# Optimization experiments

Measured on AMD Instinct MI355X. Metric: run time of the kernel, lower is better.

Reference implementation:

```python
import jax, jax.numpy as jnp
import numpy as np

B, S, H = 64, 2048, 1024

def setup_inputs() -> dict:
    key = jax.random.key(0)
    k1, k2 = jax.random.split(key)
    enc_output = jax.random.normal(k1, (B, S, H), dtype=jnp.float32)
    h_n = jax.random.normal(k2, (B, H), dtype=jnp.float32)
    return {"enc_output": enc_output, "h_n": h_n}

def reference(enc_output, h_n):
    # dec_output: [B, 1, H]
    dec_output = h_n[:, None, :]
    # scores: [B, 1, S] = dec_output @ enc_output^T
    scores = jnp.einsum('bqh,bsh->bqs', dec_output, enc_output)
    attn = jax.nn.softmax(scores, axis=2)  # softmax over S
    # context: [B, 1, H] = attn @ enc_output
    context = jnp.einsum('bqs,bsh->bqh', attn, enc_output)
    # concat decoder state and attention context: [B, 1, 2H]
    return jnp.concatenate((dec_output, context), axis=2)
```

## Files before the change

kernel.cpp:

```cpp
#include <hip/hip_runtime.h>
#include <math.h>


#define BB 64
#define SS 2048
#define HH 1024
#define NCHUNK 32
#define SCHUNK (SS / NCHUNK)
#define NWAVE 4
#define RUN (SCHUNK / NWAVE)

typedef float fvec4 __attribute__((ext_vector_type(4)));

#define WS_ML_OFF ((size_t)BB * NCHUNK * HH)

__global__ __launch_bounds__(256) void attn_partial_kernel(
    const float* __restrict__ enc, const float* __restrict__ hn,
    float* __restrict__ ws)
{
    const int blk   = blockIdx.x;
    const int b     = blk >> 5;
    const int chunk = blk & (NCHUNK - 1);
    const int tid   = threadIdx.x;
    const int wave  = tid >> 6;
    const int lane  = tid & 63;

    const fvec4* hn4 = (const fvec4*)(hn + (size_t)b * HH);
    fvec4 h4[4];
#pragma unroll
    for (int j = 0; j < 4; ++j) h4[j] = hn4[j * 64 + lane];

    const fvec4* enc4 = (const fvec4*)(enc + (size_t)b * SS * HH);

    float m = -INFINITY;
    float l = 0.0f;
    fvec4 acc[4];
#pragma unroll
    for (int j = 0; j < 4; ++j) acc[j] = (fvec4)(0.f, 0.f, 0.f, 0.f);

    const int rowbase = chunk * SCHUNK + wave * RUN;
    const int start   = (blk * 53 + wave * 29) & (RUN - 1);

    for (int i = 0; i < RUN; ++i) {
        const int r = rowbase + ((start + i) & (RUN - 1));
        const fvec4* row = enc4 + (size_t)r * (HH / 4);
        fvec4 e[4];
#pragma unroll
        for (int j = 0; j < 4; ++j)
            e[j] = __builtin_nontemporal_load(&row[j * 64 + lane]);

        float d = 0.0f;
#pragma unroll
        for (int j = 0; j < 4; ++j) {
            d += e[j].x * h4[j].x + e[j].y * h4[j].y
               + e[j].z * h4[j].z + e[j].w * h4[j].w;
        }
#pragma unroll
        for (int off = 32; off > 0; off >>= 1)
            d += __shfl_xor(d, off, 64);

        if (d <= m) {
            const float p = __expf(d - m);
            l += p;
#pragma unroll
            for (int j = 0; j < 4; ++j) {
                acc[j].x = fmaf(p, e[j].x, acc[j].x);
                acc[j].y = fmaf(p, e[j].y, acc[j].y);
                acc[j].z = fmaf(p, e[j].z, acc[j].z);
                acc[j].w = fmaf(p, e[j].w, acc[j].w);
            }
        } else {
            const float sc = __expf(m - d);
            l = fmaf(l, sc, 1.0f);
            m = d;
#pragma unroll
            for (int j = 0; j < 4; ++j) {
                acc[j].x = fmaf(acc[j].x, sc, e[j].x);
                acc[j].y = fmaf(acc[j].y, sc, e[j].y);
                acc[j].z = fmaf(acc[j].z, sc, e[j].z);
                acc[j].w = fmaf(acc[j].w, sc, e[j].w);
            }
        }
    }

    __shared__ float s_m[NWAVE];
    __shared__ float s_l[NWAVE];
    __shared__ float s_acc[NWAVE][HH];

#pragma unroll
    for (int j = 0; j < 4; ++j)
        ((fvec4*)s_acc[wave])[j * 64 + lane] = acc[j];
    if (lane == 0) { s_m[wave] = m; s_l[wave] = l; }
    __syncthreads();

    float M = fmaxf(fmaxf(s_m[0], s_m[1]), fmaxf(s_m[2], s_m[3]));
    float sc2[NWAVE];
    float L = 0.0f;
#pragma unroll
    for (int w = 0; w < NWAVE; ++w) {
        sc2[w] = __expf(s_m[w] - M);
        L += s_l[w] * sc2[w];
    }

    fvec4 ctx = (fvec4)(0.f, 0.f, 0.f, 0.f);
#pragma unroll
    for (int w = 0; w < NWAVE; ++w) {
        fvec4 a = ((const fvec4*)s_acc[w])[tid];
        ctx.x += sc2[w] * a.x;  ctx.y += sc2[w] * a.y;
        ctx.z += sc2[w] * a.z;  ctx.w += sc2[w] * a.w;
    }
    ((fvec4*)(ws + (size_t)blk * HH))[tid] = ctx;
    if (tid == 0) {
        ws[WS_ML_OFF + (size_t)blk * 2 + 0] = M;
        ws[WS_ML_OFF + (size_t)blk * 2 + 1] = L;
    }
}

__global__ __launch_bounds__(256) void attn_final_kernel(
    const float* __restrict__ hn, const float* __restrict__ ws,
    float* __restrict__ out)
{
    const int b   = blockIdx.x;
    const int tid = threadIdx.x;
    const float* ml = ws + WS_ML_OFF + (size_t)b * NCHUNK * 2;

    float M = -INFINITY;
#pragma unroll
    for (int c = 0; c < NCHUNK; ++c) M = fmaxf(M, ml[c * 2]);

    float sc[NCHUNK];
    float T = 0.0f;
#pragma unroll
    for (int c = 0; c < NCHUNK; ++c) {
        sc[c] = __expf(ml[c * 2] - M);
        T += sc[c] * ml[c * 2 + 1];
    }
    const float invT = 1.0f / T;

    fvec4 ctx = (fvec4)(0.f, 0.f, 0.f, 0.f);
#pragma unroll
    for (int c = 0; c < NCHUNK; ++c) {
        fvec4 a = ((const fvec4*)(ws + (size_t)(b * NCHUNK + c) * HH))[tid];
        ctx.x += sc[c] * a.x;  ctx.y += sc[c] * a.y;
        ctx.z += sc[c] * a.z;  ctx.w += sc[c] * a.w;
    }
    ctx.x *= invT; ctx.y *= invT; ctx.z *= invT; ctx.w *= invT;

    const fvec4 dec = ((const fvec4*)(hn + (size_t)b * HH))[tid];
    fvec4* o = (fvec4*)(out + (size_t)b * 2 * HH);
    o[tid]            = dec;
    o[tid + (HH / 4)] = ctx;
}

extern "C" void kernel_launch(void* const* d_in, const int* in_sizes, int n_in,
                              void* d_out, int out_size, void* d_ws, size_t ws_size,
                              hipStream_t stream) {
    const float* enc = (const float*)d_in[0];
    const float* hn  = (const float*)d_in[1];
    float* out = (float*)d_out;
    float* ws  = (float*)d_ws;

    attn_partial_kernel<<<dim3(BB * NCHUNK), dim3(256), 0, stream>>>(enc, hn, ws);
    attn_final_kernel<<<dim3(BB), dim3(256), 0, stream>>>(hn, ws, out);
}
```

Baseline: 659.2 us.

## Stream encoder rows through LDS with async global_load_lds multi-stage pipeline

Replaces the per-row nontemporal register loads with a 4-deep per-wave software pipeline that uses global_load_lds to copy encoder rows straight into shared memory, waiting on vmcnt before each row is consumed. This keeps several row loads in flight per wave so memory latency overlaps the dot product and online-softmax work. It also cuts the chunk count from 32 to 8, giving fewer, longer blocks with less partial workspace traffic but fewer blocks overall. It drops the staggered start offsets and needs 64KB of LDS per block, which limits occupancy.

```diff
diff --git a/kernel.cpp b/kernel.cpp
--- a/kernel.cpp
+++ b/kernel.cpp
@@ -5,21 +5,78 @@
 #define BB 64
 #define SS 2048
 #define HH 1024
-#define NCHUNK 32
+#define NCHUNK 8
 #define SCHUNK (SS / NCHUNK)
 #define NWAVE 4
 #define RUN (SCHUNK / NWAVE)
+#define DEPTH 4
 
 typedef float fvec4 __attribute__((ext_vector_type(4)));
 
 #define WS_ML_OFF ((size_t)BB * NCHUNK * HH)
 
+#define WAITVM(n) do { asm volatile("s_waitcnt vmcnt(" #n ")" ::: "memory"); \
+                       __builtin_amdgcn_sched_barrier(0); } while (0)
+
+#define STAGE(rowi, slot) do {                                               \
+    const float* g_ = gbase + (size_t)(rowi) * HH + lane * 4;                \
+    float* l_ = lbase + (slot) * HH;                                         \
+    _Pragma("unroll")                                                        \
+    for (int j_ = 0; j_ < 4; ++j_)                                           \
+        __builtin_amdgcn_global_load_lds(                                    \
+            (const __attribute__((address_space(1))) void*)(g_ + j_ * 256),  \
+            (__attribute__((address_space(3))) void*)(l_ + j_ * 256),        \
+            16, 0, 0);                                                       \
+} while (0)
+
+#define CONSUME(slot) do {                                                   \
+    const fvec4* eb_ = (const fvec4*)(lbase + (slot) * HH);                  \
+    fvec4 e_[4];                                                             \
+    _Pragma("unroll")                                                        \
+    for (int j_ = 0; j_ < 4; ++j_) e_[j_] = eb_[j_ * 64 + lane];             \
+    float d_ = 0.0f;                                                         \
+    _Pragma("unroll")                                                        \
+    for (int j_ = 0; j_ < 4; ++j_) {                                         \
+        d_ += e_[j_].x * h4[j_].x + e_[j_].y * h4[j_].y                      \
+            + e_[j_].z * h4[j_].z + e_[j_].w * h4[j_].w;                     \
+    }                                                                        \
+    _Pragma("unroll")                                                        \
+    for (int off_ = 32; off_ > 0; off_ >>= 1)                                \
+        d_ += __shfl_xor(d_, off_, 64);                                      \
+    if (d_ <= m) {                    \
+        const float p_ = __expf(d_ - m);                                     \
+        l += p_;                                                             \
+        _Pragma("unroll")                                                    \
+        for (int j_ = 0; j_ < 4; ++j_) {                                     \
+            acc[j_].x = fmaf(p_, e_[j_].x, acc[j_].x);                       \
+            acc[j_].y = fmaf(p_, e_[j_].y, acc[j_].y);                       \
+            acc[j_].z = fmaf(p_, e_[j_].z, acc[j_].z);                       \
+            acc[j_].w = fmaf(p_, e_[j_].w, acc[j_].w);                       \
+        }                                                                    \
+    } else {                                   \
+        const float sc_ = __expf(m - d_);       \
+        l = fmaf(l, sc_, 1.0f);                                              \
+        m = d_;                                                              \
+        _Pragma("unroll")                                                    \
+        for (int j_ = 0; j_ < 4; ++j_) {                                     \
+            acc[j_].x = fmaf(acc[j_].x, sc_, e_[j_].x);                      \
+            acc[j_].y = fmaf(acc[j_].y, sc_, e_[j_].y);                      \
+            acc[j_].z = fmaf(acc[j_].z, sc_, e_[j_].z);                      \
+            acc[j_].w = fmaf(acc[j_].w, sc_, e_[j_].w);                      \
+        }                                                                    \
+    }                                                                        \
+} while (0)
+
 __global__ __launch_bounds__(256) void attn_partial_kernel(
     const float* __restrict__ enc, const float* __restrict__ hn,
     float* __restrict__ ws)
 {
+    __shared__ float smem[NWAVE * DEPTH * HH];
+    __shared__ float s_m[NWAVE];
+    __shared__ float s_l[NWAVE];
+
     const int blk   = blockIdx.x;
-    const int b     = blk >> 5;
+    const int b     = blk >> 3;
     const int chunk = blk & (NCHUNK - 1);
     const int tid   = threadIdx.x;
     const int wave  = tid >> 6;
@@ -30,7 +87,9 @@
 #pragma unroll
     for (int j = 0; j < 4; ++j) h4[j] = hn4[j * 64 + lane];
 
-    const fvec4* enc4 = (const fvec4*)(enc + (size_t)b * SS * HH);
+    const float* gbase = enc + (size_t)b * SS * HH
+                       + (size_t)(chunk * SCHUNK + wave * RUN) * HH;
+    float* lbase = smem + wave * DEPTH * HH;
 
     float m = -INFINITY;
     float l = 0.0f;
@@ -38,55 +97,20 @@
 #pragma unroll
     for (int j = 0; j < 4; ++j) acc[j] = (fvec4)(0.f, 0.f, 0.f, 0.f);
 
-    const int rowbase = chunk * SCHUNK + wave * RUN;
-    const int start   = (blk * 53 + wave * 29) & (RUN - 1);
+    STAGE(0, 0); STAGE(1, 1); STAGE(2, 2); STAGE(3, 3);
 
-    for (int i = 0; i < RUN; ++i) {
-        const int r = rowbase + ((start + i) & (RUN - 1));
-        const fvec4* row = enc4 + (size_t)r * (HH / 4);
-        fvec4 e[4];
-#pragma unroll
-        for (int j = 0; j < 4; ++j)
-            e[j] = __builtin_nontemporal_load(&row[j * 64 + lane]);
+    for (int i = 0; i < RUN - DEPTH; ++i) {
+        WAITVM(12);
+        CONSUME(i & 3);
+        STAGE(i + DEPTH, i & 3);
+    }
+    WAITVM(12); CONSUME((RUN - 4) & 3);
+    WAITVM(8);  CONSUME((RUN - 3) & 3);
+    WAITVM(4);  CONSUME((RUN - 2) & 3);
+    WAITVM(0);  CONSUME((RUN - 1) & 3);
 
-        float d = 0.0f;
-#pragma unroll
-        for (int j = 0; j < 4; ++j) {
-            d += e[j].x * h4[j].x + e[j].y * h4[j].y
-               + e[j].z * h4[j].z + e[j].w * h4[j].w;
-        }
-#pragma unroll
-        for (int off = 32; off > 0; off >>= 1)
-            d += __shfl_xor(d, off, 64);
-
-        if (d <= m) {
-            const float p = __expf(d - m);
-            l += p;
-#pragma unroll
-            for (int j = 0; j < 4; ++j) {
-                acc[j].x = fmaf(p, e[j].x, acc[j].x);
-                acc[j].y = fmaf(p, e[j].y, acc[j].y);
-                acc[j].z = fmaf(p, e[j].z, acc[j].z);
-                acc[j].w = fmaf(p, e[j].w, acc[j].w);
-            }
-        } else {
-            const float sc = __expf(m - d);
-            l = fmaf(l, sc, 1.0f);
-            m = d;
-#pragma unroll
-            for (int j = 0; j < 4; ++j) {
-                acc[j].x = fmaf(acc[j].x, sc, e[j].x);
-                acc[j].y = fmaf(acc[j].y, sc, e[j].y);
-                acc[j].z = fmaf(acc[j].z, sc, e[j].z);
-                acc[j].w = fmaf(acc[j].w, sc, e[j].w);
-            }
-        }
-    }
-
-    __shared__ float s_m[NWAVE];
-    __shared__ float s_l[NWAVE];
-    __shared__ float s_acc[NWAVE][HH];
-
+    __syncthreads();
+    float (*s_acc)[HH] = (float (*)[HH])smem;
 #pragma unroll
     for (int j = 0; j < 4; ++j)
         ((fvec4*)s_acc[wave])[j * 64 + lane] = acc[j];
```

Result: slower. 684.4 us (+3.8%).
